# Kernel optimization log

Hardware: AMD Instinct MI355X
Metric: run time of the kernel (lower is better)

The kernel has to match this reference:

```python
import jax, jax.numpy as jnp
import numpy as np

N, B, T, F_IN, H1, H2 = 69, 32, 1024, 8, 32, 16


def cal_adj_norm(adj):
    # adj_norm = D^-1/2 (A + I) D^-1/2
    n = adj.shape[0]
    adj_ = adj + jnp.eye(n, dtype=adj.dtype)
    d = jnp.sum(adj_, axis=1)
    d_is = d ** -0.5
    return adj_ * d_is[:, None] * d_is[None, :]


def setup_inputs() -> dict:
    key = jax.random.key(0)
    k1, k2, k3, k4 = jax.random.split(key, 4)
    x = jax.random.normal(k1, (N, B, T, F_IN), dtype=jnp.float32)
    a = jax.random.uniform(k2, (N, N), dtype=jnp.float32)
    adj = ((a + a.T) > 1.4).astype(jnp.float32)
    W1 = jax.random.normal(k3, (F_IN, H1), dtype=jnp.float32)
    W2 = jax.random.normal(k4, (H1, H2), dtype=jnp.float32)
    return {"x": x, "adj": adj, "W1": W1, "W2": W2}


def reference(x, adj, W1, W2):
    adj_n = cal_adj_norm(adj)                      # [N, N]
    xb = jnp.transpose(x, (1, 2, 0, 3))            # [B, T, N, F_in]
    # layer 1: relu( adj_n @ x @ W1 ), batched over (B, T)
    h = jax.nn.relu(jnp.einsum('nm,btmf->btnf', adj_n, xb) @ W1)   # [B, T, N, H1]
    # layer 2: sigmoid( adj_n @ h @ W2 )
    out = jax.nn.sigmoid(jnp.einsum('nm,btmf->btnf', adj_n, h) @ W2)  # [B, T, N, H2]
    return out
```

## Files before the change

kernel.cpp:

```cpp
#include <hip/hip_runtime.h>
#include <math.h>

#define N_NODES 69
#define MP      80
#define KP      96
#define BT_TOTAL 32768
#define F_IN    8
#define H1      32
#define H2      16

#define TBT     8
#define BLOCK   256

#define ZPITCH3 104
#define HBPITCH 40

typedef __attribute__((ext_vector_type(8))) short bf16x8;
typedef __attribute__((ext_vector_type(4))) float f32x4;
typedef __attribute__((ext_vector_type(2), aligned(8)))  unsigned u32x2;
typedef __attribute__((ext_vector_type(4), aligned(16))) unsigned u32x4;

typedef bf16x8 __attribute__((may_alias)) bf16x8_a;
typedef u32x2  __attribute__((may_alias)) u32x2_a;
typedef u32x4  __attribute__((may_alias)) u32x4_a;

__device__ __forceinline__ unsigned short f2bf(float f) {
    unsigned u = __float_as_uint(f);
    return (unsigned short)((u + 0x7FFFu + ((u >> 16) & 1u)) >> 16);
}
__device__ __forceinline__ float bf2f(unsigned short h) {
    return __uint_as_float(((unsigned)h) << 16);
}

__global__ void setup_kernel(const float* __restrict__ adj,
                             unsigned short* __restrict__ adjh,
                             unsigned short* __restrict__ adjl)
{
    __shared__ float dinv[N_NODES];
    const int tid = threadIdx.x;
    if (tid < N_NODES) {
        float s = 1.0f;
        for (int j = 0; j < N_NODES; ++j) s += adj[tid * N_NODES + j];
        dinv[tid] = rsqrtf(s);
    }
    __syncthreads();
    for (int idx = tid; idx < MP * KP; idx += BLOCK) {
        const int n = idx / KP, m = idx % KP;
        float v = 0.0f;
        if (n < N_NODES && m < N_NODES) {
            float a = adj[n * N_NODES + m] + (n == m ? 1.0f : 0.0f);
            v = a * dinv[n] * dinv[m];
        }
        unsigned short h = f2bf(v);
        adjh[idx] = h;
        adjl[idx] = f2bf(v - bf2f(h));
    }
}

__global__ __launch_bounds__(BLOCK, 5) void gcn_kernel(
    const float* __restrict__ x,
    const unsigned short* __restrict__ adjh,
    const unsigned short* __restrict__ adjl,
    const float* __restrict__ W1g,
    const float* __restrict__ W2g,
    float* __restrict__ out)
{
    __shared__ unsigned short Zt[128 * ZPITCH3];
    __shared__ unsigned short Hb_s[4][16 * HBPITCH];

    const int tid  = threadIdx.x;
    const int lane = tid & 63;
    const int wv   = tid >> 6;
    const int quad = lane >> 4;
    const int l16  = lane & 15;
    const int bt0  = blockIdx.x * TBT;

    {
        const int row = wv * 32 + (lane >> 1);
        const int col = 80 + (lane & 1) * 8;
        *(u32x4_a*)&Zt[row * ZPITCH3 + col] = (u32x4){0u, 0u, 0u, 0u};
    }

    const int btg = bt0 + wv * 2 + (l16 >> 3);
    const int fl  = l16 & 7;

    f32x4 acc[5] = {};
#pragma unroll
    for (int kt = 0; kt < 3; ++kt) {
        union AF { unsigned u[4]; bf16x8 v; } ah, al;
#pragma unroll
        for (int p = 0; p < 4; ++p) {
            const int m0 = kt * 32 + quad * 8 + 2 * p;
            const int m1 = m0 + 1;
            float x0 = 0.0f, x1 = 0.0f;
            if (kt < 2) {
                x0 = x[(size_t)m0 * 262144 + btg * 8 + fl];
                x1 = x[(size_t)m1 * 262144 + btg * 8 + fl];
            } else {
                if (m0 < N_NODES) x0 = x[(size_t)m0 * 262144 + btg * 8 + fl];
                if (m1 < N_NODES) x1 = x[(size_t)m1 * 262144 + btg * 8 + fl];
            }
            const unsigned short h0 = f2bf(x0), h1 = f2bf(x1);
            ah.u[p] = (unsigned)h0 | ((unsigned)h1 << 16);
            const unsigned short g0 = f2bf(x0 - bf2f(h0));
            const unsigned short g1 = f2bf(x1 - bf2f(h1));
            al.u[p] = (unsigned)g0 | ((unsigned)g1 << 16);
        }
#pragma unroll
        for (int nt = 0; nt < 5; ++nt) {
            const int boff = (nt * 16 + l16) * KP + kt * 32 + quad * 8;
            const bf16x8 bh = *(const bf16x8_a*)(adjh + boff);
            const bf16x8 bl = *(const bf16x8_a*)(adjl + boff);
            acc[nt] = __builtin_amdgcn_mfma_f32_16x16x32_bf16(ah.v, bh, acc[nt], 0, 0, 0);
            acc[nt] = __builtin_amdgcn_mfma_f32_16x16x32_bf16(ah.v, bl, acc[nt], 0, 0, 0);
            acc[nt] = __builtin_amdgcn_mfma_f32_16x16x32_bf16(al.v, bh, acc[nt], 0, 0, 0);
        }
    }

    bf16x8 w1f[2][2] = {};
    {
        const int fb0 = quad * 4;
        const int fb1 = (quad - 2) * 4;
#pragma unroll
        for (int ht = 0; ht < 2; ++ht) {
#pragma unroll
            for (int j = 0; j < 4; ++j) {
                const float a0 = (quad < 2)  ? W1g[(fb0 + j) * H1 + ht * 16 + l16] : 0.0f;
                const float a1 = (quad >= 2) ? W1g[(fb1 + j) * H1 + ht * 16 + l16] : 0.0f;
                w1f[0][ht][j] = (short)f2bf(a0);
                w1f[1][ht][j] = (short)f2bf(a1);
            }
        }
    }
    bf16x8 w2f;
#pragma unroll
    for (int j = 0; j < 8; ++j)
        w2f[j] = (short)f2bf(W2g[(quad * 8 + j) * H2 + l16]);

    unsigned short* Hb = Hb_s[wv];

    auto do_bt = [&](const f32x4& h0, const f32x4& h1, int btl, int nt) {
#pragma unroll
        for (int reg = 0; reg < 4; ++reg) {
            const int row = quad * 4 + reg;
            Hb[row * HBPITCH + l16]      = f2bf(fmaxf(h0[reg], 0.f));
            Hb[row * HBPITCH + 16 + l16] = f2bf(fmaxf(h1[reg], 0.f));
        }
        const bf16x8 a2 = *(const bf16x8_a*)&Hb[l16 * HBPITCH + quad * 8];
        f32x4 zk = {0.f, 0.f, 0.f, 0.f};
        zk = __builtin_amdgcn_mfma_f32_16x16x32_bf16(a2, w2f, zk, 0, 0, 0);
        const unsigned z0 = (unsigned)f2bf(zk[0]) | ((unsigned)f2bf(zk[1]) << 16);
        const unsigned z1 = (unsigned)f2bf(zk[2]) | ((unsigned)f2bf(zk[3]) << 16);
        *(u32x2_a*)&Zt[(btl * 16 + l16) * ZPITCH3 + nt * 16 + quad * 4] = (u32x2){z0, z1};
    };

#pragma unroll
    for (int nt = 0; nt < 5; ++nt) {
        const unsigned d0 = (unsigned)f2bf(acc[nt][0]) | ((unsigned)f2bf(acc[nt][1]) << 16);
        const unsigned d1 = (unsigned)f2bf(acc[nt][2]) | ((unsigned)f2bf(acc[nt][3]) << 16);
        union AF { unsigned u[4]; bf16x8 v; } af;
        af.u[0] = d0; af.u[1] = d1; af.u[2] = d0; af.u[3] = d1;

        const f32x4 zz = {0.f, 0.f, 0.f, 0.f};
        f32x4 hL0 = __builtin_amdgcn_mfma_f32_16x16x32_bf16(af.v, w1f[0][0], zz, 0, 0, 0);
        f32x4 hL1 = __builtin_amdgcn_mfma_f32_16x16x32_bf16(af.v, w1f[0][1], zz, 0, 0, 0);
        f32x4 hH0 = __builtin_amdgcn_mfma_f32_16x16x32_bf16(af.v, w1f[1][0], zz, 0, 0, 0);
        f32x4 hH1 = __builtin_amdgcn_mfma_f32_16x16x32_bf16(af.v, w1f[1][1], zz, 0, 0, 0);

        do_bt(hL0, hL1, wv * 2 + 0, nt);
        do_bt(hH0, hH1, wv * 2 + 1, nt);
    }

    __syncthreads();

    bf16x8 bz[2][3];
#pragma unroll
    for (int c = 0; c < 2; ++c)
#pragma unroll
        for (int kt = 0; kt < 3; ++kt)
            bz[c][kt] = *(const bf16x8_a*)
                &Zt[((wv * 2 + c) * 16 + l16) * ZPITCH3 + kt * 32 + quad * 8];

#pragma unroll
    for (int mt = 0; mt < 5; ++mt) {
        bf16x8 am[3];
#pragma unroll
        for (int kt = 0; kt < 3; ++kt)
            am[kt] = *(const bf16x8_a*)&adjh[(mt * 16 + l16) * KP + kt * 32 + quad * 8];
#pragma unroll
        for (int c = 0; c < 2; ++c) {
            f32x4 a3 = {0.f, 0.f, 0.f, 0.f};
#pragma unroll
            for (int kt = 0; kt < 3; ++kt)
                a3 = __builtin_amdgcn_mfma_f32_16x16x32_bf16(am[kt], bz[c][kt], a3, 0, 0, 0);
            const int ct3 = wv * 2 + c;
            float* outc = out + ((size_t)(bt0 + ct3) * N_NODES) * H2 + l16;
#pragma unroll
            for (int reg = 0; reg < 4; ++reg) {
                const int n = mt * 16 + quad * 4 + reg;
                if (n < N_NODES) {
                    const float v = 1.0f / (1.0f + __expf(-a3[reg]));
                    outc[n * H2] = v;
                }
            }
        }
    }
}

extern "C" void kernel_launch(void* const* d_in, const int* in_sizes, int n_in,
                              void* d_out, int out_size, void* d_ws, size_t ws_size,
                              hipStream_t stream) {
    const float* x   = (const float*)d_in[0];
    const float* adj = (const float*)d_in[1];
    const float* W1  = (const float*)d_in[2];
    const float* W2  = (const float*)d_in[3];
    float* out = (float*)d_out;

    unsigned short* adjh = (unsigned short*)d_ws;
    unsigned short* adjl = adjh + MP * KP;

    setup_kernel<<<1, BLOCK, 0, stream>>>(adj, adjh, adjl);
    gcn_kernel<<<BT_TOTAL / TBT, BLOCK, 0, stream>>>(x, adjh, adjl, W1, W2, out);
}
```

Baseline: 267.4 us.

## Keep adjacency hi fragments in registers and batch x loads upfront

```diff
diff --git a/kernel.cpp b/kernel.cpp
--- a/kernel.cpp
+++ b/kernel.cpp
@@ -57,7 +57,7 @@
     }
 }
 
-__global__ __launch_bounds__(BLOCK, 5) void gcn_kernel(
+__global__ __launch_bounds__(BLOCK, 4) void gcn_kernel(
     const float* __restrict__ x,
     const unsigned short* __restrict__ adjh,
     const unsigned short* __restrict__ adjl,
@@ -66,7 +66,7 @@
     float* __restrict__ out)
 {
     __shared__ unsigned short Zt[128 * ZPITCH3];
-    __shared__ unsigned short Hb_s[4][16 * HBPITCH];
+    __shared__ unsigned short Hb_s[4][2][16 * HBPITCH];
 
     const int tid  = threadIdx.x;
     const int lane = tid & 63;
@@ -81,39 +81,55 @@
         *(u32x4_a*)&Zt[row * ZPITCH3 + col] = (u32x4){0u, 0u, 0u, 0u};
     }
 
+    bf16x8 ahf[15];
+#pragma unroll
+    for (int t = 0; t < 15; ++t) {
+        const int nt = t / 3, kt = t % 3;
+        ahf[t] = *(const bf16x8_a*)&adjh[(nt * 16 + l16) * KP + kt * 32 + quad * 8];
+    }
+
     const int btg = bt0 + wv * 2 + (l16 >> 3);
     const int fl  = l16 & 7;
 
-    f32x4 acc[5] = {};
+    float xv[3][8];
 #pragma unroll
     for (int kt = 0; kt < 3; ++kt) {
-        union AF { unsigned u[4]; bf16x8 v; } ah, al;
 #pragma unroll
         for (int p = 0; p < 4; ++p) {
             const int m0 = kt * 32 + quad * 8 + 2 * p;
             const int m1 = m0 + 1;
-            float x0 = 0.0f, x1 = 0.0f;
             if (kt < 2) {
-                x0 = x[(size_t)m0 * 262144 + btg * 8 + fl];
-                x1 = x[(size_t)m1 * 262144 + btg * 8 + fl];
+                xv[kt][2 * p]     = x[(size_t)m0 * 262144 + btg * 8 + fl];
+                xv[kt][2 * p + 1] = x[(size_t)m1 * 262144 + btg * 8 + fl];
             } else {
-                if (m0 < N_NODES) x0 = x[(size_t)m0 * 262144 + btg * 8 + fl];
-                if (m1 < N_NODES) x1 = x[(size_t)m1 * 262144 + btg * 8 + fl];
+                xv[kt][2 * p]     = (m0 < N_NODES) ? x[(size_t)m0 * 262144 + btg * 8 + fl] : 0.0f;
+                xv[kt][2 * p + 1] = (m1 < N_NODES) ? x[(size_t)m1 * 262144 + btg * 8 + fl] : 0.0f;
             }
+        }
+    }
+
+    f32x4 acc[5] = {};
+#pragma unroll
+    for (int kt = 0; kt < 3; ++kt) {
+        union AF { unsigned u[4]; bf16x8 v; } ah, al;
+#pragma unroll
+        for (int p = 0; p < 4; ++p) {
+            const float x0 = xv[kt][2 * p], x1 = xv[kt][2 * p + 1];
             const unsigned short h0 = f2bf(x0), h1 = f2bf(x1);
             ah.u[p] = (unsigned)h0 | ((unsigned)h1 << 16);
             const unsigned short g0 = f2bf(x0 - bf2f(h0));
             const unsigned short g1 = f2bf(x1 - bf2f(h1));
             al.u[p] = (unsigned)g0 | ((unsigned)g1 << 16);
         }
+        bf16x8 alf[5];
+#pragma unroll
+        for (int nt = 0; nt < 5; ++nt)
+            alf[nt] = *(const bf16x8_a*)&adjl[(nt * 16 + l16) * KP + kt * 32 + quad * 8];
 #pragma unroll
         for (int nt = 0; nt < 5; ++nt) {
-            const int boff = (nt * 16 + l16) * KP + kt * 32 + quad * 8;
-            const bf16x8 bh = *(const bf16x8_a*)(adjh + boff);
-            const bf16x8 bl = *(const bf16x8_a*)(adjl + boff);
-            acc[nt] = __builtin_amdgcn_mfma_f32_16x16x32_bf16(ah.v, bh, acc[nt], 0, 0, 0);
-            acc[nt] = __builtin_amdgcn_mfma_f32_16x16x32_bf16(ah.v, bl, acc[nt], 0, 0, 0);
-            acc[nt] = __builtin_amdgcn_mfma_f32_16x16x32_bf16(al.v, bh, acc[nt], 0, 0, 0);
+            acc[nt] = __builtin_amdgcn_mfma_f32_16x16x32_bf16(ah.v, ahf[nt * 3 + kt], acc[nt], 0, 0, 0);
+            acc[nt] = __builtin_amdgcn_mfma_f32_16x16x32_bf16(ah.v, alf[nt], acc[nt], 0, 0, 0);
+            acc[nt] = __builtin_amdgcn_mfma_f32_16x16x32_bf16(al.v, ahf[nt * 3 + kt], acc[nt], 0, 0, 0);
         }
     }
 
@@ -137,9 +153,8 @@
     for (int j = 0; j < 8; ++j)
         w2f[j] = (short)f2bf(W2g[(quad * 8 + j) * H2 + l16]);
 
-    unsigned short* Hb = Hb_s[wv];
-
-    auto do_bt = [&](const f32x4& h0, const f32x4& h1, int btl, int nt) {
+    auto do_bt = [&](const f32x4& h0, const f32x4& h1, int btl, int nt,
+                     unsigned short* Hb) {
 #pragma unroll
         for (int reg = 0; reg < 4; ++reg) {
             const int row = quad * 4 + reg;
@@ -167,8 +182,8 @@
         f32x4 hH0 = __builtin_amdgcn_mfma_f32_16x16x32_bf16(af.v, w1f[1][0], zz, 0, 0, 0);
         f32x4 hH1 = __builtin_amdgcn_mfma_f32_16x16x32_bf16(af.v, w1f[1][1], zz, 0, 0, 0);
 
-        do_bt(hL0, hL1, wv * 2 + 0, nt);
-        do_bt(hH0, hH1, wv * 2 + 1, nt);
+        do_bt(hL0, hL1, wv * 2 + 0, nt, &Hb_s[wv][0][0]);
+        do_bt(hH0, hH1, wv * 2 + 1, nt, &Hb_s[wv][1][0]);
     }
 
     __syncthreads();
@@ -183,16 +198,12 @@
 
 #pragma unroll
     for (int mt = 0; mt < 5; ++mt) {
-        bf16x8 am[3];
-#pragma unroll
-        for (int kt = 0; kt < 3; ++kt)
-            am[kt] = *(const bf16x8_a*)&adjh[(mt * 16 + l16) * KP + kt * 32 + quad * 8];
 #pragma unroll
         for (int c = 0; c < 2; ++c) {
             f32x4 a3 = {0.f, 0.f, 0.f, 0.f};
 #pragma unroll
             for (int kt = 0; kt < 3; ++kt)
-                a3 = __builtin_amdgcn_mfma_f32_16x16x32_bf16(am[kt], bz[c][kt], a3, 0, 0, 0);
+                a3 = __builtin_amdgcn_mfma_f32_16x16x32_bf16(ahf[mt * 3 + kt], bz[c][kt], a3, 0, 0, 0);
             const int ct3 = wv * 2 + c;
             float* outc = out + ((size_t)(bt0 + ct3) * N_NODES) * H2 + l16;
 #pragma unroll
```

Result: faster. 259.2 us (-3.1%).
